# Kernel tuning notes

Hardware: AMD Instinct MI355X
Metric: run time of the kernel (lower is better)

The kernel has to match this reference:

```python
import jax, jax.numpy as jnp
import numpy as np

EPS = 1e-12  # torch f.normalize eps


def _rms_norm(x, g):
    # f.normalize(x, dim=1) * g * sqrt(C): L2-normalize over channel dim
    c = x.shape[1]
    n = jnp.maximum(jnp.linalg.norm(x, axis=1, keepdims=True), EPS)
    return x / n * g * (c ** 0.5)


def setup_inputs() -> dict:
    key = jax.random.key(0)
    ks = jax.random.split(key, 5)
    b, dim, H, W = 32, 256, 64, 64
    heads, dim_head, num_mem = 4, 32, 4
    hidden = heads * dim_head
    return {
        "x": jax.random.normal(ks[0], (b, dim, H, W), dtype=jnp.float32),
        "g1": jnp.ones((1, dim, 1, 1), dtype=jnp.float32),
        "mem_kv": jax.random.normal(ks[1], (2, heads, dim_head, num_mem), dtype=jnp.float32),
        "w_qkv": jax.random.normal(ks[2], (3 * hidden, dim), dtype=jnp.float32) * (1.0 / np.sqrt(dim)),
        "w_out": jax.random.normal(ks[3], (dim, hidden), dtype=jnp.float32) * (1.0 / np.sqrt(hidden)),
        "b_out": jnp.zeros((dim,), dtype=jnp.float32),
        "g2": jnp.ones((1, dim, 1, 1), dtype=jnp.float32),
    }


def reference(x, g1, mem_kv, w_qkv, w_out, b_out, g2):
    b, c, H, W = x.shape
    _, heads, dim_head, num_mem = mem_kv.shape
    n = H * W
    scale = dim_head ** -0.5

    xn = _rms_norm(x, g1)
    # 1x1 conv qkv projection: [b, 3*hidden, H, W]
    qkv = jnp.einsum('oc,bchw->bohw', w_qkv, xn)
    hidden = heads * dim_head
    q, k, v = jnp.split(qkv, 3, axis=1)
    # b (h d) x y -> b h d (x y)
    q = q.reshape(b, heads, dim_head, n)
    k = k.reshape(b, heads, dim_head, n)
    v = v.reshape(b, heads, dim_head, n)

    mk = jnp.broadcast_to(mem_kv[0], (b, heads, dim_head, num_mem))
    mv = jnp.broadcast_to(mem_kv[1], (b, heads, dim_head, num_mem))
    k = jnp.concatenate([mk, k], axis=-1)
    v = jnp.concatenate([mv, v], axis=-1)

    q = jax.nn.softmax(q, axis=-2) * scale  # softmax over head dim d
    k = jax.nn.softmax(k, axis=-1)          # softmax over sequence n

    context = jnp.einsum('bhdn,bhen->bhde', k, v)   # [b,h,d,e]
    out = jnp.einsum('bhde,bhdn->bhen', context, q)  # [b,h,e,n]
    out = out.reshape(b, hidden, H, W)

    o = jnp.einsum('oc,bchw->bohw', w_out, out) + b_out[None, :, None, None]
    return _rms_norm(o, g2)
```

## Files before the change

### kernel.cpp

```cpp
#include <hip/hip_runtime.h>
#include <math.h>

#define CC   256
#define HW   4096
#define OC3  384
#define HID  128
#define DH   32
#define NM   4
#define NPART 8
#define SCALE 0.17677669529663688f

typedef __bf16 bf16x8 __attribute__((ext_vector_type(8)));
typedef float  f32x4  __attribute__((ext_vector_type(4)));

__device__ __forceinline__ ushort f2bf(float x) {
    union { float f; unsigned u; } v; v.f = x;
    unsigned r = v.u + 0x7fffu + ((v.u >> 16) & 1u);
    return (ushort)(r >> 16);
}
__device__ __forceinline__ float bf2f(ushort b) {
    union { unsigned u; float f; } v; v.u = ((unsigned)b) << 16; return v.f;
}
__device__ __forceinline__ void g2l16(const void* g, void* l) {
    __builtin_amdgcn_global_load_lds(
        (const __attribute__((address_space(1))) void*)g,
        (__attribute__((address_space(3))) void*)l, 16, 0, 0);
}

__global__ void k_prep(const float* __restrict__ wqkv, const float* __restrict__ g1,
                       const float* __restrict__ wout,
                       ushort* __restrict__ wq2t, ushort* __restrict__ woutt) {
    int o = blockIdx.x, t = threadIdx.x;
    wq2t[(size_t)o * CC + t] = f2bf(wqkv[(size_t)o * CC + t] * g1[t] * 16.0f);
    if (o < CC && t < HID) woutt[(size_t)o * HID + t] = f2bf(wout[(size_t)o * HID + t]);
}

__global__ __launch_bounds__(256) void k_xn(const float* __restrict__ x,
                                            ushort* __restrict__ xnT) {
    __shared__ float xt[256 * 33];
    __shared__ float ps[8 * 33];
    __shared__ float invn[32];
    int tid = threadIdx.x;
    int pix0 = blockIdx.x * 32;
    int b = pix0 >> 12, hw0 = pix0 & 4095;
    int p = tid & 31, cg = tid >> 5;
    const float* xb = x + (size_t)b * CC * HW + hw0;
    #pragma unroll 4
    for (int step = 0; step < 32; ++step) {
        int c = step * 8 + cg;
        xt[c * 33 + p] = xb[(size_t)c * HW + p];
    }
    __syncthreads();
    float s = 0.f;
    #pragma unroll 8
    for (int i = 0; i < 32; ++i) { float v = xt[(cg * 32 + i) * 33 + p]; s += v * v; }
    ps[cg * 33 + p] = s;
    __syncthreads();
    if (tid < 32) {
        float t = 0.f;
        #pragma unroll
        for (int g = 0; g < 8; ++g) t += ps[g * 33 + tid];
        invn[tid] = 1.0f / fmaxf(sqrtf(t), 1e-12f);
    }
    __syncthreads();
    float inv = invn[p];
    ushort* dst = xnT + ((size_t)(pix0 + p)) * CC + cg * 32;
    #pragma unroll
    for (int q = 0; q < 4; ++q) {
        uint4 pk; ushort* o8 = (ushort*)&pk;
        #pragma unroll
        for (int i = 0; i < 8; ++i) o8[i] = f2bf(xt[(cg * 32 + q * 8 + i) * 33 + p] * inv);
        *(uint4*)&dst[q * 8] = pk;
    }
}

__global__ __launch_bounds__(256) void k_qkv(const ushort* __restrict__ wq2t,
        const ushort* __restrict__ xnT, ushort* __restrict__ qkv) {
    __shared__ ushort As[128 * 32];
    __shared__ ushort Bs[128 * 32];
    int tid = threadIdx.x;
    int m0 = blockIdx.x * 128;
    int p0 = blockIdx.y * 128;
    int b  = blockIdx.z;
    int lane = tid & 63, wid = tid >> 6;
    int l15 = tid & 15, quad = (tid >> 4) & 3;
    int wm = wid >> 1, wn = wid & 1;
    int rsub = lane >> 2, csub = (lane & 3) * 8;
    const ushort* Ab = wq2t + (size_t)m0 * CC;
    const ushort* Bb = xnT + ((size_t)(b * HW + p0)) * CC;
    f32x4 acc[4][4];
    #pragma unroll
    for (int i = 0; i < 4; ++i)
        #pragma unroll
        for (int j = 0; j < 4; ++j) acc[i][j] = (f32x4){0.f, 0.f, 0.f, 0.f};
    for (int k0 = 0; k0 < CC; k0 += 32) {
        __syncthreads();
        #pragma unroll
        for (int q = 0; q < 2; ++q) {
            int rw = wid * 32 + q * 16;
            g2l16(Ab + (size_t)(rw + rsub) * CC + k0 + csub, &As[rw * 32]);
            g2l16(Bb + (size_t)(rw + rsub) * CC + k0 + csub, &Bs[rw * 32]);
        }
        __syncthreads();
        bf16x8 af[4], bfr[4];
        #pragma unroll
        for (int mt = 0; mt < 4; ++mt)
            af[mt] = *(const bf16x8*)&As[(wm * 64 + mt * 16 + l15) * 32 + quad * 8];
        #pragma unroll
        for (int nt = 0; nt < 4; ++nt)
            bfr[nt] = *(const bf16x8*)&Bs[(wn * 64 + nt * 16 + l15) * 32 + quad * 8];
        #pragma unroll
        for (int mt = 0; mt < 4; ++mt)
            #pragma unroll
            for (int nt = 0; nt < 4; ++nt)
                acc[mt][nt] = __builtin_amdgcn_mfma_f32_16x16x32_bf16(
                                  af[mt], bfr[nt], acc[mt][nt], 0, 0, 0);
    }
    #pragma unroll
    for (int mt = 0; mt < 4; ++mt) {
        int o = m0 + wm * 64 + mt * 16 + quad * 4;
        #pragma unroll
        for (int nt = 0; nt < 4; ++nt) {
            int pix = p0 + wn * 64 + nt * 16 + l15;
            ushort* dst = qkv + ((size_t)(b * OC3 + o)) * HW + pix;
            #pragma unroll
            for (int r = 0; r < 4; ++r) dst[(size_t)r * HW] = f2bf(acc[mt][nt][r]);
        }
    }
}

__global__ void k_ksoft(const ushort* __restrict__ qkv, const float* __restrict__ memkv,
                        float* __restrict__ kmaxb, float* __restrict__ rsumb) {
    int row = blockIdx.x * 4 + (threadIdx.x >> 6);
    int lane = threadIdx.x & 63;
    int b = row >> 7, hd = row & 127;
    const ushort* kp = qkv + ((size_t)(b * OC3 + HID + hd)) * HW;
    float m = -1e30f;
    for (int i = lane; i < HW; i += 64) m = fmaxf(m, bf2f(kp[i]));
    #pragma unroll
    for (int s = 1; s < 64; s <<= 1) m = fmaxf(m, __shfl_xor(m, s));
    const float* mk = memkv + hd * NM;
    #pragma unroll
    for (int j = 0; j < NM; ++j) m = fmaxf(m, mk[j]);
    float s = 0.f;
    for (int i = lane; i < HW; i += 64) s += __expf(bf2f(kp[i]) - m);
    #pragma unroll
    for (int t = 1; t < 64; t <<= 1) s += __shfl_xor(s, t);
    #pragma unroll
    for (int j = 0; j < NM; ++j) s += __expf(mk[j] - m);
    if (lane == 0) { kmaxb[row] = m; rsumb[row] = 1.0f / s; }
}

__global__ __launch_bounds__(256) void k_ctx(const ushort* __restrict__ qkv,
        const float* __restrict__ memkv, const float* __restrict__ kmaxb,
        const float* __restrict__ rsumb, float* __restrict__ ctxp) {
    __shared__ float kl[DH][65];
    __shared__ float vl[DH][65];
    __shared__ float red[256 * 33];
    int tid = threadIdx.x;
    int bh = blockIdx.x;
    int part = blockIdx.y;
    int b = bh >> 2, h = bh & 3;
    const ushort* kp = qkv + ((size_t)(b * OC3 + HID + h * DH)) * HW + part * 512;
    const ushort* vp = qkv + ((size_t)(b * OC3 + 2 * HID + h * DH)) * HW + part * 512;
    int slot = tid & 31, nng = tid >> 5;
    int d0 = (slot >> 2) * 4, e0 = (slot & 3) * 8;
    int rowbase = bh * DH;
    float acc[4][8];
    #pragma unroll
    for (int i = 0; i < 4; ++i)
        #pragma unroll
        for (int j = 0; j < 8; ++j) acc[i][j] = 0.f;
    for (int n0 = 0; n0 < 512; n0 += 64) {
        __syncthreads();
        #pragma unroll
        for (int q = 0; q < 8; ++q) {
            int idx = tid + q * 256;
            int r = idx >> 6, nn = idx & 63;
            float kraw = bf2f(kp[(size_t)r * HW + n0 + nn]);
            kl[r][nn] = __expf(kraw - kmaxb[rowbase + r]) * rsumb[rowbase + r];
            vl[r][nn] = bf2f(vp[(size_t)r * HW + n0 + nn]);
        }
        __syncthreads();
        #pragma unroll 2
        for (int t = 0; t < 8; ++t) {
            int nn = nng * 8 + t;
            float kv[4], vv[8];
            #pragma unroll
            for (int i = 0; i < 4; ++i) kv[i] = kl[d0 + i][nn];
            #pragma unroll
            for (int j = 0; j < 8; ++j) vv[j] = vl[e0 + j][nn];
            #pragma unroll
            for (int i = 0; i < 4; ++i)
                #pragma unroll
                for (int j = 0; j < 8; ++j) acc[i][j] += kv[i] * vv[j];
        }
    }
    __syncthreads();
    #pragma unroll
    for (int i = 0; i < 4; ++i)
        #pragma unroll
        for (int j = 0; j < 8; ++j) red[tid * 33 + i * 8 + j] = acc[i][j];
    __syncthreads();
    #pragma unroll
    for (int q = 0; q < 4; ++q) {
        int o = tid * 4 + q;
        int d = o >> 5, e = o & 31;
        int sl = (d >> 2) * 4 + (e >> 3);
        int k = (d & 3) * 8 + (e & 7);
        float s = 0.f;
        #pragma unroll
        for (int g = 0; g < 8; ++g) s += red[(g * 32 + sl) * 33 + k];
        if (part == 0) {
            float km = kmaxb[rowbase + d], rsm = rsumb[rowbase + d];
            #pragma unroll
            for (int m = 0; m < NM; ++m) {
                float kw = __expf(memkv[(h * DH + d) * NM + m] - km) * rsm;
                s += kw * memkv[512 + (h * DH + e) * NM + m];
            }
        }
        ctxp[(size_t)part * 131072 + (size_t)bh * 1024 + o] = s;
    }
}

__global__ __launch_bounds__(256) void k_attn_final(const ushort* __restrict__ qkv,
        const float* __restrict__ ctxp, const ushort* __restrict__ woutt,
        const float* __restrict__ bout, const float* __restrict__ g2,
        float* __restrict__ y) {
    __shared__ __align__(16) char smem[51712];
    ushort* qs   = (ushort*)smem;
    ushort* outT = (ushort*)smem;
    ushort* sq   = (ushort*)(smem + 17408);
    ushort* Asm  = (ushort*)(smem + 17408);
    ushort* ctxT = (ushort*)(smem + 34816);
    float*  red  = (float*)(smem + 45056);
    float*  invs = (float*)(smem + 49408);
    float*  bl   = (float*)(smem + 49664);
    float*  gl   = (float*)(smem + 50688);
    int tid = threadIdx.x;
    int b = blockIdx.y;
    int hwb = blockIdx.x * 64;
    int lane = tid & 63, wid = tid >> 6;
    int l15 = tid & 15, quad = (tid >> 4) & 3;
    bl[tid] = bout[tid];
    gl[tid] = g2[tid];

    const ushort* qp = qkv + ((size_t)b * OC3) * HW + hwb;
    #pragma unroll
    for (int i = 0; i < 8; ++i) {
        int flat = i * 1024 + tid * 4;
        int r = flat >> 6, p = flat & 63;
        *(uint2*)&qs[r * 68 + p] = *(const uint2*)&qp[(size_t)r * HW + p];
    }
    {
        int rem = tid & 63;
        int d = rem >> 1, e0 = (rem & 1) * 16;
        const float* cb = ctxp + (size_t)b * 4096 + wid * 1024 + d * 32 + e0;
        float cv[16];
        #pragma unroll
        for (int i = 0; i < 16; ++i) cv[i] = 0.f;
        #pragma unroll
        for (int part = 0; part < NPART; ++part)
            #pragma unroll
            for (int i = 0; i < 16; ++i) cv[i] += cb[(size_t)part * 131072 + i];
        #pragma unroll
        for (int i = 0; i < 16; ++i)
            ctxT[(wid * 32 + e0 + i) * 40 + d] = f2bf(cv[i]);
    }
    __syncthreads();

    {
        float vd[32];
        float m = -1e30f;
        #pragma unroll
        for (int dd = 0; dd < 32; ++dd) {
            float v = bf2f(qs[(wid * 32 + dd) * 68 + lane]);
            vd[dd] = v; m = fmaxf(m, v);
        }
        float s = 0.f;
        #pragma unroll
        for (int dd = 0; dd < 32; ++dd) { float e = __expf(vd[dd] - m); vd[dd] = e; s += e; }
        float r_ = SCALE / s;
        #pragma unroll
        for (int qI = 0; qI < 4; ++qI) {
            uint4 pk; ushort* o8 = (ushort*)&pk;
            #pragma unroll
            for (int i = 0; i < 8; ++i) o8[i] = f2bf(vd[qI * 8 + i] * r_);
            *(uint4*)&sq[lane * 136 + wid * 32 + qI * 8] = pk;
        }
    }
    __syncthreads();

    f32x4 acc3[4][2];
    #pragma unroll
    for (int i = 0; i < 4; ++i)
        #pragma unroll
        for (int j = 0; j < 2; ++j) acc3[i][j] = (f32x4){0.f, 0.f, 0.f, 0.f};
    {
        bf16x8 a3[4], b3[2];
        #pragma unroll
        for (int mt = 0; mt < 4; ++mt)
            a3[mt] = *(const bf16x8*)&sq[(mt * 16 + l15) * 136 + wid * 32 + quad * 8];
        #pragma unroll
        for (int nt = 0; nt < 2; ++nt)
            b3[nt] = *(const bf16x8*)&ctxT[(wid * 32 + nt * 16 + l15) * 40 + quad * 8];
        #pragma unroll
        for (int mt = 0; mt < 4; ++mt)
            #pragma unroll
            for (int nt = 0; nt < 2; ++nt)
                acc3[mt][nt] = __builtin_amdgcn_mfma_f32_16x16x32_bf16(
                                   a3[mt], b3[nt], acc3[mt][nt], 0, 0, 0);
    }
    __syncthreads();
    #pragma unroll
    for (int mt = 0; mt < 4; ++mt)
        #pragma unroll
        for (int nt = 0; nt < 2; ++nt)
            #pragma unroll
            for (int r = 0; r < 4; ++r)
                outT[(mt * 16 + quad * 4 + r) * 136 + wid * 32 + nt * 16 + l15] =
                    f2bf(acc3[mt][nt][r]);

    f32x4 acc[4][4];
    #pragma unroll
    for (int i = 0; i < 4; ++i)
        #pragma unroll
        for (int j = 0; j < 4; ++j) acc[i][j] = (f32x4){0.f, 0.f, 0.f, 0.f};
    int rsub = lane >> 2, csub = (lane & 3) * 8;
    for (int k0 = 0; k0 < HID; k0 += 32) {
        __syncthreads();
        #pragma unroll
        for (int q = 0; q < 4; ++q) {
            int rw = wid * 64 + q * 16;
            g2l16(woutt + (size_t)(rw + rsub) * HID + k0 + csub, &Asm[rw * 32]);
        }
        __syncthreads();
        bf16x8 af[4], bfr[4];
        #pragma unroll
        for (int mt = 0; mt < 4; ++mt)
            af[mt] = *(const bf16x8*)&Asm[(wid * 64 + mt * 16 + l15) * 32 + quad * 8];
        #pragma unroll
        for (int nt = 0; nt < 4; ++nt)
            bfr[nt] = *(const bf16x8*)&outT[(nt * 16 + l15) * 136 + k0 + quad * 8];
        #pragma unroll
        for (int mt = 0; mt < 4; ++mt)
            #pragma unroll
            for (int nt = 0; nt < 4; ++nt)
                acc[mt][nt] = __builtin_amdgcn_mfma_f32_16x16x32_bf16(
                                  af[mt], bfr[nt], acc[mt][nt], 0, 0, 0);
    }

    float part[4] = {0.f, 0.f, 0.f, 0.f};
    #pragma unroll
    for (int mt = 0; mt < 4; ++mt)
        #pragma unroll
        for (int r = 0; r < 4; ++r) {
            int oc = wid * 64 + mt * 16 + quad * 4 + r;
            float bo = bl[oc];
            #pragma unroll
            for (int nt = 0; nt < 4; ++nt) {
                float v = acc[mt][nt][r] + bo;
                acc[mt][nt][r] = v;
                part[nt] += v * v;
            }
        }
    __syncthreads();
    #pragma unroll
    for (int nt = 0; nt < 4; ++nt)
        red[(nt * 16 + l15) * 17 + wid * 4 + quad] = part[nt];
    __syncthreads();
    if (tid < 64) {
        float s = 0.f;
        #pragma unroll
        for (int g = 0; g < 16; ++g) s += red[tid * 17 + g];
        invs[tid] = 1.0f / fmaxf(sqrtf(s), 1e-12f);
    }
    __syncthreads();
    #pragma unroll
    for (int mt = 0; mt < 4; ++mt)
        #pragma unroll
        for (int nt = 0; nt < 4; ++nt) {
            int pix = nt * 16 + l15;
            float iv = invs[pix];
            #pragma unroll
            for (int r = 0; r < 4; ++r) {
                int oc = wid * 64 + mt * 16 + quad * 4 + r;
                y[((size_t)(b * CC + oc)) * HW + hwb + pix] = acc[mt][nt][r] * iv * gl[oc] * 16.0f;
            }
        }
}

extern "C" void kernel_launch(void* const* d_in, const int* in_sizes, int n_in,
                              void* d_out, int out_size, void* d_ws, size_t ws_size,
                              hipStream_t stream) {
    const float* x     = (const float*)d_in[0];
    const float* g1    = (const float*)d_in[1];
    const float* memkv = (const float*)d_in[2];
    const float* wqkv  = (const float*)d_in[3];
    const float* wout  = (const float*)d_in[4];
    const float* bout  = (const float*)d_in[5];
    const float* g2    = (const float*)d_in[6];
    float* y = (float*)d_out;

    char* w = (char*)d_ws;
    ushort* wq2t  = (ushort*)w;  w += (size_t)OC3 * CC * 2;
    ushort* woutt = (ushort*)w;  w += (size_t)CC * HID * 2;
    float*  kmaxb = (float*)w;   w += 4096 * 4;
    float*  rsumb = (float*)w;   w += 4096 * 4;
    float*  ctxp  = (float*)w;   w += (size_t)NPART * 131072 * 4;
    ushort* xnT   = (ushort*)w;  w += (size_t)32 * HW * CC * 2;
    ushort* qkv   = (ushort*)w;  w += (size_t)32 * OC3 * HW * 2;

    k_prep      <<<dim3(384),       dim3(256), 0, stream>>>(wqkv, g1, wout, wq2t, woutt);
    k_xn        <<<dim3(4096),      dim3(256), 0, stream>>>(x, xnT);
    k_qkv       <<<dim3(3, 32, 32), dim3(256), 0, stream>>>(wq2t, xnT, qkv);
    k_ksoft     <<<dim3(1024),      dim3(256), 0, stream>>>(qkv, memkv, kmaxb, rsumb);
    k_ctx       <<<dim3(128, 8),    dim3(256), 0, stream>>>(qkv, memkv, kmaxb, rsumb, ctxp);
    k_attn_final<<<dim3(64, 32),    dim3(256), 0, stream>>>(qkv, ctxp, woutt, bout, g2, y);
}
```

Measured before the change: 422.2 us.

## Fold attention context into output projection per batch and swizzle QKV block order

Adds a small per-batch kernel that sums the partial contexts and multiplies them into the output projection weights, giving a fused per-batch weight W2 = Wout·ctx. The final kernel then needs only the q softmax followed by one GEMM against W2. This drops the per-tile context reduction and the extra context MFMA stage, at the cost of one more launch and a per-batch weight buffer. Separately, the QKV GEMM's block index is remapped so neighbouring workgroups are spread across XCDs/tiles.

```diff
diff --git a/kernel.cpp b/kernel.cpp
--- a/kernel.cpp
+++ b/kernel.cpp
@@ -79,9 +79,12 @@
     __shared__ ushort As[128 * 32];
     __shared__ ushort Bs[128 * 32];
     int tid = threadIdx.x;
-    int m0 = blockIdx.x * 128;
-    int p0 = blockIdx.y * 128;
-    int b  = blockIdx.z;
+    int lin = blockIdx.x + 3 * (blockIdx.y + 32 * blockIdx.z);
+    int swz = (lin & 7) * 384 + (lin >> 3);
+    int m0 = (swz % 3) * 128;
+    int t_ = swz / 3;
+    int p0 = (t_ & 31) * 128;
+    int b  = t_ >> 5;
     int lane = tid & 63, wid = tid >> 6;
     int l15 = tid & 15, quad = (tid >> 4) & 3;
     int wm = wid >> 1, wn = wid & 1;
@@ -223,20 +226,66 @@
     }
 }
 
-__global__ __launch_bounds__(256) void k_attn_final(const ushort* __restrict__ qkv,
-        const float* __restrict__ ctxp, const ushort* __restrict__ woutt,
-        const float* __restrict__ bout, const float* __restrict__ g2,
-        float* __restrict__ y) {
-    __shared__ __align__(16) char smem[51712];
-    ushort* qs   = (ushort*)smem;
-    ushort* outT = (ushort*)smem;
-    ushort* sq   = (ushort*)(smem + 17408);
-    ushort* Asm  = (ushort*)(smem + 17408);
-    ushort* ctxT = (ushort*)(smem + 34816);
-    float*  red  = (float*)(smem + 45056);
-    float*  invs = (float*)(smem + 49408);
-    float*  bl   = (float*)(smem + 49664);
-    float*  gl   = (float*)(smem + 50688);
+__global__ __launch_bounds__(256) void k_w2(const float* __restrict__ ctxp,
+        const ushort* __restrict__ woutt, ushort* __restrict__ W2) {
+    __shared__ ushort ctxb[4 * 32 * 40];
+    int tid = threadIdx.x, b = blockIdx.x;
+    int wid = tid >> 6;
+    int l15 = tid & 15, quad = (tid >> 4) & 3;
+    #pragma unroll
+    for (int j = 0; j < 16; ++j) {
+        int idx = tid + j * 256;
+        float s = 0.f;
+        #pragma unroll
+        for (int p = 0; p < NPART; ++p)
+            s += ctxp[(size_t)p * 131072 + (size_t)b * 4096 + idx];
+        int h = idx >> 10, d = (idx >> 5) & 31, e = idx & 31;
+        ctxb[(h * 32 + d) * 40 + e] = f2bf(s);
+    }
+    __syncthreads();
+    #pragma unroll
+    for (int h = 0; h < 4; ++h) {
+        f32x4 acc[4][2];
+        #pragma unroll
+        for (int i = 0; i < 4; ++i)
+            #pragma unroll
+            for (int j = 0; j < 2; ++j) acc[i][j] = (f32x4){0.f, 0.f, 0.f, 0.f};
+        bf16x8 af[4], bfr[2];
+        #pragma unroll
+        for (int mt = 0; mt < 4; ++mt)
+            af[mt] = *(const bf16x8*)&woutt[(size_t)(wid * 64 + mt * 16 + l15) * HID
+                                            + h * DH + quad * 8];
+        #pragma unroll
+        for (int nt = 0; nt < 2; ++nt)
+            bfr[nt] = *(const bf16x8*)&ctxb[(h * 32 + nt * 16 + l15) * 40 + quad * 8];
+        #pragma unroll
+        for (int mt = 0; mt < 4; ++mt)
+            #pragma unroll
+            for (int nt = 0; nt < 2; ++nt)
+                acc[mt][nt] = __builtin_amdgcn_mfma_f32_16x16x32_bf16(
+                                  af[mt], bfr[nt], acc[mt][nt], 0, 0, 0);
+        #pragma unroll
+        for (int mt = 0; mt < 4; ++mt)
+            #pragma unroll
+            for (int nt = 0; nt < 2; ++nt)
+                #pragma unroll
+                for (int r = 0; r < 4; ++r) {
+                    int oc = wid * 64 + mt * 16 + quad * 4 + r;
+                    int d  = nt * 16 + l15;
+                    W2[((size_t)b * CC + oc) * HID + h * DH + d] = f2bf(acc[mt][nt][r]);
+                }
+    }
+}
+
+__global__ __launch_bounds__(256) void k_final(const ushort* __restrict__ qkv,
+        const ushort* __restrict__ W2, const float* __restrict__ bout,
+        const float* __restrict__ g2, float* __restrict__ y) {
+    __shared__ __align__(16) ushort sq[64 * 136];
+    __shared__ __align__(16) ushort Ws[256 * 32];
+    __shared__ float red[64 * 17];
+    __shared__ float invs[64];
+    __shared__ float bl[256];
+    __shared__ float gl[256];
     int tid = threadIdx.x;
     int b = blockIdx.y;
     int hwb = blockIdx.x * 64;
@@ -245,81 +294,27 @@
     bl[tid] = bout[tid];
     gl[tid] = g2[tid];
 
-    const ushort* qp = qkv + ((size_t)b * OC3) * HW + hwb;
-    #pragma unroll
-    for (int i = 0; i < 8; ++i) {
-        int flat = i * 1024 + tid * 4;
-        int r = flat >> 6, p = flat & 63;
-        *(uint2*)&qs[r * 68 + p] = *(const uint2*)&qp[(size_t)r * HW + p];
-    }
     {
-        int rem = tid & 63;
-        int d = rem >> 1, e0 = (rem & 1) * 16;
-        const float* cb = ctxp + (size_t)b * 4096 + wid * 1024 + d * 32 + e0;
-        float cv[16];
-        #pragma unroll
-        for (int i = 0; i < 16; ++i) cv[i] = 0.f;
-        #pragma unroll
-        for (int part = 0; part < NPART; ++part)
-            #pragma unroll
-            for (int i = 0; i < 16; ++i) cv[i] += cb[(size_t)part * 131072 + i];
-        #pragma unroll
-        for (int i = 0; i < 16; ++i)
-            ctxT[(wid * 32 + e0 + i) * 40 + d] = f2bf(cv[i]);
-    }
-    __syncthreads();
-
-    {
+        const ushort* qp = qkv + ((size_t)b * OC3 + wid * DH) * HW + hwb + lane;
         float vd[32];
         float m = -1e30f;
         #pragma unroll
-        for (int dd = 0; dd < 32; ++dd) {
-            float v = bf2f(qs[(wid * 32 + dd) * 68 + lane]);
-            vd[dd] = v; m = fmaxf(m, v);
+        for (int d = 0; d < 32; ++d) {
+            float v = bf2f(qp[(size_t)d * HW]);
+            vd[d] = v; m = fmaxf(m, v);
         }
         float s = 0.f;
         #pragma unroll
-        for (int dd = 0; dd < 32; ++dd) { float e = __expf(vd[dd] - m); vd[dd] = e; s += e; }
+        for (int d = 0; d < 32; ++d) { float e = __expf(vd[d] - m); vd[d] = e; s += e; }
         float r_ = SCALE / s;
         #pragma unroll
-        for (int qI = 0; qI < 4; ++qI) {
+        for (int q8 = 0; q8 < 4; ++q8) {
             uint4 pk; ushort* o8 = (ushort*)&pk;
             #pragma unroll
-            for (int i = 0; i < 8; ++i) o8[i] = f2bf(vd[qI * 8 + i] * r_);
-            *(uint4*)&sq[lane * 136 + wid * 32 + qI * 8] = pk;
-        }
-    }
-    __syncthreads();
-
-    f32x4 acc3[4][2];
-    #pragma unroll
-    for (int i = 0; i < 4; ++i)
-        #pragma unroll
-        for (int j = 0; j < 2; ++j) acc3[i][j] = (f32x4){0.f, 0.f, 0.f, 0.f};
-    {
-        bf16x8 a3[4], b3[2];
-        #pragma unroll
-        for (int mt = 0; mt < 4; ++mt)
-            a3[mt] = *(const bf16x8*)&sq[(mt * 16 + l15) * 136 + wid * 32 + quad * 8];
-        #pragma unroll
-        for (int nt = 0; nt < 2; ++nt)
-            b3[nt] = *(const bf16x8*)&ctxT[(wid * 32 + nt * 16 + l15) * 40 + quad * 8];
-        #pragma unroll
-        for (int mt = 0; mt < 4; ++mt)
-            #pragma unroll
-            for (int nt = 0; nt < 2; ++nt)
-                acc3[mt][nt] = __builtin_amdgcn_mfma_f32_16x16x32_bf16(
-                                   a3[mt], b3[nt], acc3[mt][nt], 0, 0, 0);
-    }
-    __syncthreads();
-    #pragma unroll
-    for (int mt = 0; mt < 4; ++mt)
-        #pragma unroll
-        for (int nt = 0; nt < 2; ++nt)
-            #pragma unroll
-            for (int r = 0; r < 4; ++r)
-                outT[(mt * 16 + quad * 4 + r) * 136 + wid * 32 + nt * 16 + l15] =
-                    f2bf(acc3[mt][nt][r]);
+            for (int i = 0; i < 8; ++i) o8[i] = f2bf(vd[q8 * 8 + i] * r_);
+            *(uint4*)&sq[lane * 136 + wid * DH + q8 * 8] = pk;
+        }
+    }
 
     f32x4 acc[4][4];
     #pragma unroll
@@ -327,21 +322,22 @@
         #pragma unroll
         for (int j = 0; j < 4; ++j) acc[i][j] = (f32x4){0.f, 0.f, 0.f, 0.f};
     int rsub = lane >> 2, csub = (lane & 3) * 8;
+    const ushort* W2b = W2 + (size_t)b * CC * HID;
     for (int k0 = 0; k0 < HID; k0 += 32) {
         __syncthreads();
         #pragma unroll
         for (int q = 0; q < 4; ++q) {
             int rw = wid * 64 + q * 16;
-            g2l16(woutt + (size_t)(rw + rsub) * HID + k0 + csub, &Asm[rw * 32]);
+            g2l16(W2b + (size_t)(rw + rsub) * HID + k0 + csub, &Ws[rw * 32]);
         }
         __syncthreads();
         bf16x8 af[4], bfr[4];
         #pragma unroll
         for (int mt = 0; mt < 4; ++mt)
-            af[mt] = *(const bf16x8*)&Asm[(wid * 64 + mt * 16 + l15) * 32 + quad * 8];
+            af[mt] = *(const bf16x8*)&Ws[(wid * 64 + mt * 16 + l15) * 32 + quad * 8];
         #pragma unroll
         for (int nt = 0; nt < 4; ++nt)
-            bfr[nt] = *(const bf16x8*)&outT[(nt * 16 + l15) * 136 + k0 + quad * 8];
+            bfr[nt] = *(const bf16x8*)&sq[(nt * 16 + l15) * 136 + k0 + quad * 8];
         #pragma unroll
         for (int mt = 0; mt < 4; ++mt)
             #pragma unroll
@@ -408,13 +404,15 @@
     float*  kmaxb = (float*)w;   w += 4096 * 4;
     float*  rsumb = (float*)w;   w += 4096 * 4;
     float*  ctxp  = (float*)w;   w += (size_t)NPART * 131072 * 4;
+    ushort* W2    = (ushort*)w;  w += (size_t)32 * CC * HID * 2;
     ushort* xnT   = (ushort*)w;  w += (size_t)32 * HW * CC * 2;
     ushort* qkv   = (ushort*)w;  w += (size_t)32 * OC3 * HW * 2;
 
-    k_prep      <<<dim3(384),       dim3(256), 0, stream>>>(wqkv, g1, wout, wq2t, woutt);
-    k_xn        <<<dim3(4096),      dim3(256), 0, stream>>>(x, xnT);
-    k_qkv       <<<dim3(3, 32, 32), dim3(256), 0, stream>>>(wq2t, xnT, qkv);
-    k_ksoft     <<<dim3(1024),      dim3(256), 0, stream>>>(qkv, memkv, kmaxb, rsumb);
-    k_ctx       <<<dim3(128, 8),    dim3(256), 0, stream>>>(qkv, memkv, kmaxb, rsumb, ctxp);
-    k_attn_final<<<dim3(64, 32),    dim3(256), 0, stream>>>(qkv, ctxp, woutt, bout, g2, y);
-}
+    k_prep  <<<dim3(384),       dim3(256), 0, stream>>>(wqkv, g1, wout, wq2t, woutt);
+    k_xn    <<<dim3(4096),      dim3(256), 0, stream>>>(x, xnT);
+    k_qkv   <<<dim3(3, 32, 32), dim3(256), 0, stream>>>(wq2t, xnT, qkv);
+    k_ksoft <<<dim3(1024),      dim3(256), 0, stream>>>(qkv, memkv, kmaxb, rsumb);
+    k_ctx   <<<dim3(128, 8),    dim3(256), 0, stream>>>(qkv, memkv, kmaxb, rsumb, ctxp);
+    k_w2    <<<dim3(32),        dim3(256), 0, stream>>>(ctxp, woutt, W2);
+    k_final <<<dim3(64, 32),    dim3(256), 0, stream>>>(qkv, W2, bout, g2, y);
+}
```

New measurement: 399.3 us. -5.4%, faster.
